# Kernel tuning notes

Hardware: AMD Instinct MI355X
Metric: run time of the kernel (lower is better)

The kernel has to match this reference:

```python
import jax, jax.numpy as jnp
import numpy as np

N_FEAT = 512
N_HEAD = 8
CONTEXT_SIZES = (31, 61)
HEADS_PER_SCALE = N_HEAD // len(CONTEXT_SIZES)  # 4
B, T = 4, 2048


def _windows(v, cs):
    """Gather overlapping local windows (faithful to chunkwise with N_c=1).
    v: [B, T, D] -> [B, T, cs, D], zero-padded at both ends by (cs-1)//2."""
    Bv, Tv, D = v.shape
    half = (cs - 1) // 2
    vp = jnp.pad(v, ((0, 0), (half, half), (0, 0)))
    idx = jnp.arange(Tv)[:, None] + jnp.arange(cs)[None, :]  # [T, cs]
    return vp[:, idx, :]


def setup_inputs() -> dict:
    key0 = jax.random.key(0)
    ks = jax.random.split(key0, 12)
    s = 0.02
    inp = {
        "query": jax.random.normal(ks[0], (B, T, N_FEAT), jnp.float32),
        "key": jax.random.normal(ks[1], (B, T, N_FEAT), jnp.float32),
        "value": jax.random.normal(ks[2], (B, T, N_FEAT), jnp.float32),
        # Linear weights stored torch-style [out_features, in_features]
        "w1_0": jax.random.normal(ks[3], (N_FEAT, N_FEAT), jnp.float32) * s,
        "w1_1": jax.random.normal(ks[4], (N_FEAT, N_FEAT), jnp.float32) * s,
        "w2_0": jax.random.normal(ks[5], (HEADS_PER_SCALE * CONTEXT_SIZES[0], N_FEAT), jnp.float32) * s,
        "w2_1": jax.random.normal(ks[6], (HEADS_PER_SCALE * CONTEXT_SIZES[1], N_FEAT), jnp.float32) * s,
        "w3_0": jax.random.normal(ks[7], (N_FEAT, N_FEAT), jnp.float32) * s,
        "w3_1": jax.random.normal(ks[8], (N_FEAT, N_FEAT), jnp.float32) * s,
        "scale_weights": jnp.ones((len(CONTEXT_SIZES),), jnp.float32) / len(CONTEXT_SIZES),
        "w_out": jax.random.normal(ks[9], (N_FEAT, N_FEAT), jnp.float32) * s,
    }
    return inp


def reference(query, key, value, w1_0, w1_1, w2_0, w2_1, w3_0, w3_1, scale_weights, w_out):
    # key is unused by the original module's forward.
    Bq, Tq, Fq = query.shape
    hd = Fq // N_HEAD  # per-head dim within a scale after splitting n_feat by heads_per_scale? No:
    head_dim = Fq // HEADS_PER_SCALE  # matches original: D // heads_per_scale
    outs = []
    for (w1, w2, w3, cs) in ((w1_0, w2_0, w3_0, CONTEXT_SIZES[0]),
                             (w1_1, w2_1, w3_1, CONTEXT_SIZES[1])):
        q = query @ w1.T                      # [B,T,F]
        v = value @ w3.T                      # [B,T,F]
        logits = jax.nn.relu(q) @ w2.T        # [B,T,HS*cs]
        attn = jax.nn.softmax(logits.reshape(Bq, Tq, HEADS_PER_SCALE, cs), axis=-1)
        # local windows of v: [B,T,cs,F] -> [B,T,cs,HS,head_dim]
        vw = _windows(v, cs).reshape(Bq, Tq, cs, HEADS_PER_SCALE, head_dim)
        x = jnp.einsum('bthc,btchd->bthd', attn, vw).reshape(Bq, Tq, Fq)
        outs.append(x)
    sw = jax.nn.softmax(scale_weights)
    x = sw[0] * outs[0] + sw[1] * outs[1]
    return x @ w_out.T
```

## Files before the change

kernel.cpp:

```cpp
#include <hip/hip_runtime.h>

typedef unsigned short u16;
typedef unsigned long long u64;
typedef float floatx4 __attribute__((ext_vector_type(4)));
typedef short shortx8 __attribute__((ext_vector_type(8)));

__device__ inline u16 f2bf(float f) {
  unsigned u = __float_as_uint(f);
  u += 0x7fffu + ((u >> 16) & 1u);
  return (u16)(u >> 16);
}

__device__ __forceinline__ void gl16(const u16* g, const u16* l) {
  __builtin_amdgcn_global_load_lds(
      (const __attribute__((address_space(1))) unsigned int*)(u64)(const void*)g,
      (__attribute__((address_space(3))) unsigned int*)(unsigned)(u64)(const void*)l,
      16, 0, 0);
}

__global__ __launch_bounds__(256) void convert_all(
    const float* __restrict__ q, const float* __restrict__ v,
    const float* __restrict__ w10, const float* __restrict__ w11,
    const float* __restrict__ w30, const float* __restrict__ w31,
    const float* __restrict__ wo, const float* __restrict__ w20,
    const float* __restrict__ w21, u16* __restrict__ base) {
  size_t e = ((size_t)blockIdx.x * 256 + threadIdx.x) * 4;
  const float* src;
  u16* dst;
  size_t le;
  unsigned prows;
  if (e < 4194304ull)      { src = q;   dst = base;            le = e;            prows = 0x7fffffffu; }
  else if (e < 8388608ull) { src = v;   dst = base + 4194304;  le = e - 4194304;  prows = 0x7fffffffu; }
  else if (e < 8650752ull) { src = w10; dst = base + 8388608;  le = e - 8388608;  prows = 0x7fffffffu; }
  else if (e < 8912896ull) { src = w11; dst = base + 8650752;  le = e - 8650752;  prows = 0x7fffffffu; }
  else if (e < 9175040ull) { src = w30; dst = base + 8912896;  le = e - 8912896;  prows = 0x7fffffffu; }
  else if (e < 9437184ull) { src = w31; dst = base + 9175040;  le = e - 9175040;  prows = 0x7fffffffu; }
  else if (e < 9699328ull) { src = wo;  dst = base + 9437184;  le = e - 9437184;  prows = 0x7fffffffu; }
  else if (e < 9764864ull) { src = w20; dst = base + 9699328;  le = e - 9699328;  prows = 124; }
  else                     { src = w21; dst = base + 9764864;  le = e - 9764864;  prows = 244; }
  float4 val = make_float4(0.f, 0.f, 0.f, 0.f);
  if ((unsigned)(le >> 9) < prows) val = *(const float4*)(src + le);
  unsigned p0 = (unsigned)f2bf(val.x) | ((unsigned)f2bf(val.y) << 16);
  unsigned p1 = (unsigned)f2bf(val.z) | ((unsigned)f2bf(val.w) << 16);
  *(uint2*)(dst + le) = make_uint2(p0, p1);
}

template <int OUTBF>
__device__ __forceinline__ void gemm_core(
    const u16* __restrict__ A, int lda, const u16* __restrict__ W, int ldw,
    float* __restrict__ Cf, u16* __restrict__ Cb, int ldc, int relu,
    u16* lA, u16* lB) {
  const int tid = threadIdx.x;
  const int wave = tid >> 6, lane = tid & 63;
  const int wm = (wave >> 1) * 64, wn = (wave & 1) * 64;
  const int lr = lane & 15, kq = (lane >> 4) * 8;
  const int sr = lane >> 2, sc = (lane & 3) * 8;

  floatx4 acc[4][4];
#pragma unroll
  for (int i = 0; i < 4; ++i)
#pragma unroll
    for (int j = 0; j < 4; ++j) acc[i][j] = (floatx4){0.f, 0.f, 0.f, 0.f};

  const u16* ga0 = A + (u64)(wave * 32 + sr) * lda + sc;
  const u16* ga1 = A + (u64)(wave * 32 + 16 + sr) * lda + sc;
  const u16* gb0 = W + (u64)(wave * 32 + sr) * ldw + sc;
  const u16* gb1 = W + (u64)(wave * 32 + 16 + sr) * ldw + sc;
  u16* la0 = lA + (wave * 32) * 32;
  u16* la1 = lA + (wave * 32 + 16) * 32;
  u16* lb0 = lB + (wave * 32) * 32;
  u16* lb1 = lB + (wave * 32 + 16) * 32;

  for (int k0 = 0; k0 < 512; k0 += 32) {
    __syncthreads();
    gl16(ga0 + k0, la0);
    gl16(ga1 + k0, la1);
    gl16(gb0 + k0, lb0);
    gl16(gb1 + k0, lb1);
    __syncthreads();
    shortx8 af[4], bf8[4];
#pragma unroll
    for (int i = 0; i < 4; ++i) {
      af[i] = *(const shortx8*)&lA[(wm + i * 16 + lr) * 32 + kq];
      bf8[i] = *(const shortx8*)&lB[(wn + i * 16 + lr) * 32 + kq];
    }
#pragma unroll
    for (int mi = 0; mi < 4; ++mi)
#pragma unroll
      for (int ni = 0; ni < 4; ++ni)
        acc[mi][ni] = __builtin_amdgcn_mfma_f32_16x16x32_bf16(af[mi], bf8[ni], acc[mi][ni], 0, 0, 0);
  }
  const int er = wm + (lane >> 4) * 4;
  const int ec = wn + lr;
#pragma unroll
  for (int mi = 0; mi < 4; ++mi)
#pragma unroll
    for (int ni = 0; ni < 4; ++ni)
#pragma unroll
      for (int r = 0; r < 4; ++r) {
        float vv = acc[mi][ni][r];
        if (relu) vv = fmaxf(vv, 0.f);
        u64 off = (u64)(er + mi * 16 + r) * (u64)ldc + (u64)(ec + ni * 16);
        if (OUTBF) Cb[off] = f2bf(vv);
        else Cf[off] = vv;
      }
}

__global__ __launch_bounds__(512, 2) void k_qv8(
    const u16* __restrict__ qb, const u16* __restrict__ vb,
    const u16* __restrict__ w1, const u16* __restrict__ w3,
    u16* __restrict__ rq, u16* __restrict__ vc) {
  extern __shared__ __align__(16) u16 lds[];
  const int bid = blockIdx.x;
  const int bx = (bid & 7) * 32 + (bid >> 3);
  const bool isq = bx < 128;
  const int lb = isq ? bx : bx - 128;
  const int m0 = (lb >> 2) * 256;
  const int n0 = (lb & 3) * 256;
  const u16* __restrict__ A = isq ? qb : vb;
  const u16* __restrict__ W = isq ? w1 : w3;
  u16* __restrict__ C = isq ? rq : vc;

  const int tid = threadIdx.x;
  const int wv = tid >> 6, lane = tid & 63;
  const int wr = wv >> 2, wc = wv & 3;
  const int lr = lane & 15, kq = lane >> 4;

  const unsigned Ca = ((unsigned)((lr >> 1) & 7)) << 3;
  const unsigned afb = ((unsigned)((wr * 128 + lr) * 32 + kq * 8)) ^ Ca;
  const unsigned bfb = ((unsigned)((wc * 32 + lr) * 32 + kq * 8)) ^ Ca;

  const unsigned u0 = (unsigned)(wv * 1024 + lane * 8);
  const unsigned u1 = u0 + 512;
  const unsigned g0 = u0 ^ (((u0 >> 6) & 7) << 3);
  const unsigned g1 = u1 ^ (((u1 >> 6) & 7) << 3);
  const unsigned gA0 = (unsigned)(m0 + (int)(g0 >> 5)) * 512u + (g0 & 31);
  const unsigned gA1 = (unsigned)(m0 + (int)(g1 >> 5)) * 512u + (g1 & 31);
  const unsigned rp0 = (g0 >> 5) & 127, rp1 = (g1 >> 5) & 127;
  const unsigned gB0n0 = (unsigned)(n0 + (int)((rp0 >> 5) * 64 + (rp0 & 31))) * 512u
                         + (g0 >> 12) * 32 + (g0 & 31);
  const unsigned gB1n0 = (unsigned)(n0 + (int)((rp1 >> 5) * 64 + (rp1 & 31))) * 512u
                         + (g1 >> 12) * 32 + (g1 & 31);
  const unsigned gB0n1 = gB0n0 + 32u * 512u;
  const unsigned gB1n1 = gB1n0 + 32u * 512u;
  const unsigned wvo = (unsigned)wv * 1024u;

#define SA(d, kk, ga, gb, ko) \
  gl16(A + (ga) + (ko), lds + (d)*16384 + (kk)*8192 + wvo); \
  gl16(A + (gb) + (ko), lds + (d)*16384 + (kk)*8192 + wvo + 512)
#define SB(d, nh, ga, gb, ko) \
  gl16(W + (ga) + (ko), lds + 32768 + (d)*16384 + (nh)*8192 + wvo); \
  gl16(W + (gb) + (ko), lds + 32768 + (d)*16384 + (nh)*8192 + wvo + 512)
#define LOAD_AF(kk, d) \
  _Pragma("unroll") \
  for (int m = 0; m < 8; ++m) \
    af[m] = *(const shortx8*)&lds[(d)*16384 + (kk)*8192 + afb + (unsigned)m * 512]
#define LOAD_BF(kk, nh, d) \
  bf0 = *(const shortx8*)&lds[32768 + (d)*16384 + (nh)*8192 + (kk)*4096 + bfb]; \
  bf1 = *(const shortx8*)&lds[32768 + (d)*16384 + (nh)*8192 + (kk)*4096 + bfb + 512]
#define MFMA16(nh) \
  __builtin_amdgcn_s_setprio(1); \
  _Pragma("unroll") \
  for (int m = 0; m < 8; ++m) { \
    acc[m][(nh)*2]   = __builtin_amdgcn_mfma_f32_16x16x32_bf16(af[m], bf0, acc[m][(nh)*2], 0, 0, 0); \
    acc[m][(nh)*2+1] = __builtin_amdgcn_mfma_f32_16x16x32_bf16(af[m], bf1, acc[m][(nh)*2+1], 0, 0, 0); \
  } \
  __builtin_amdgcn_s_setprio(0)
#define BAR() \
  __builtin_amdgcn_sched_barrier(0); \
  __builtin_amdgcn_s_barrier(); \
  asm volatile("" ::: "memory"); \
  __builtin_amdgcn_sched_barrier(0)
#define WAITVM4() \
  __builtin_amdgcn_sched_barrier(0); \
  asm volatile("s_waitcnt vmcnt(4)" ::: "memory"); \
  __builtin_amdgcn_sched_barrier(0)
#define WAITVM0() \
  __builtin_amdgcn_sched_barrier(0); \
  asm volatile("s_waitcnt vmcnt(0)" ::: "memory"); \
  __builtin_amdgcn_sched_barrier(0)

  floatx4 acc[8][4];
#pragma unroll
  for (int m = 0; m < 8; ++m)
#pragma unroll
    for (int n = 0; n < 4; ++n) acc[m][n] = (floatx4){0.f, 0.f, 0.f, 0.f};
  shortx8 af[8], bf0, bf1;

  SA(0, 0, gA0, gA1, 0);
  SB(0, 0, gB0n0, gB1n0, 0);
  SA(0, 1, gA0 + 32, gA1 + 32, 0);
  SB(0, 1, gB0n1, gB1n1, 0);
  SA(1, 0, gA0, gA1, 64);
  SB(1, 0, gB0n0, gB1n0, 64);
  WAITVM4();
  BAR();

#pragma unroll 1
  for (int i = 0; i < 3; ++i) {
    const unsigned k1 = (unsigned)(2 * i + 1) * 64u;
    const unsigned k2 = k1 + 64u, k3 = k1 + 128u;
    SA(1, 1, gA0 + 32, gA1 + 32, k1);
    LOAD_AF(0, 0); LOAD_BF(0, 0, 0); MFMA16(0);
    BAR();
    SB(1, 1, gB0n1, gB1n1, k1);
    LOAD_BF(0, 1, 0); MFMA16(1);
    BAR();
    SA(0, 0, gA0, gA1, k2);
    LOAD_AF(1, 0); LOAD_BF(1, 0, 0); MFMA16(0);
    BAR();
    SB(0, 0, gB0n0, gB1n0, k2);
    LOAD_BF(1, 1, 0); MFMA16(1);
    WAITVM4();
    BAR();
    SA(0, 1, gA0 + 32, gA1 + 32, k2);
    LOAD_AF(0, 1); LOAD_BF(0, 0, 1); MFMA16(0);
    BAR();
    SB(0, 1, gB0n1, gB1n1, k2);
    LOAD_BF(0, 1, 1); MFMA16(1);
    BAR();
    SA(1, 0, gA0, gA1, k3);
    LOAD_AF(1, 1); LOAD_BF(1, 0, 1); MFMA16(0);
    BAR();
    SB(1, 0, gB0n0, gB1n0, k3);
    LOAD_BF(1, 1, 1); MFMA16(1);
    WAITVM4();
    BAR();
  }
  {
    const unsigned k1 = 448u;
    SA(1, 1, gA0 + 32, gA1 + 32, k1);
    LOAD_AF(0, 0); LOAD_BF(0, 0, 0); MFMA16(0);
    BAR();
    SB(1, 1, gB0n1, gB1n1, k1);
    LOAD_BF(0, 1, 0); MFMA16(1);
    BAR();
    LOAD_AF(1, 0); LOAD_BF(1, 0, 0); MFMA16(0);
    BAR();
    LOAD_BF(1, 1, 0); MFMA16(1);
    WAITVM0();
    BAR();
    LOAD_AF(0, 1); LOAD_BF(0, 0, 1); MFMA16(0);
    BAR();
    LOAD_BF(0, 1, 1); MFMA16(1);
    BAR();
    LOAD_AF(1, 1); LOAD_BF(1, 0, 1); MFMA16(0);
    BAR();
    LOAD_BF(1, 1, 1); MFMA16(1);
  }

  const int er0 = m0 + wr * 128 + (lane >> 4) * 4;
  const int ec0 = n0 + wc * 64 + lr;
#pragma unroll
  for (int m = 0; m < 8; ++m)
#pragma unroll
    for (int n = 0; n < 4; ++n)
#pragma unroll
      for (int r = 0; r < 4; ++r) {
        float vv = acc[m][n][r];
        if (isq) vv = fmaxf(vv, 0.f);
        C[(u64)(er0 + m * 16 + r) * 1024 + (u64)(ec0 + n * 16)] = f2bf(vv);
      }
#undef SA
#undef SB
#undef LOAD_AF
#undef LOAD_BF
#undef MFMA16
#undef BAR
#undef WAITVM4
#undef WAITVM0
}

__global__ __launch_bounds__(256, 2) void k_logits(
    const u16* __restrict__ rq, const u16* __restrict__ w20,
    const u16* __restrict__ w21, float* __restrict__ lg) {
  __shared__ __align__(16) u16 lA[128 * 32];
  __shared__ __align__(16) u16 lB[128 * 32];
  const int am = blockIdx.x * 128;
  const int y = blockIdx.y;
  const u16* A = rq + (u64)am * 1024 + (y == 0 ? 0 : 512);
  const u16* W = (y == 0) ? w20 : (w21 + (u64)(y - 1) * 128 * 512);
  float* Cf = lg + (u64)am * 384 + y * 128;
  gemm_core<0>(A, 1024, W, 512, Cf, nullptr, 384, 0, lA, lB);
}

__global__ __launch_bounds__(256, 2) void k_final(
    const u16* __restrict__ xb, const u16* __restrict__ wo,
    float* __restrict__ out) {
  __shared__ __align__(16) u16 lA[128 * 32];
  __shared__ __align__(16) u16 lB[128 * 32];
  const int am = blockIdx.x * 128, bn = blockIdx.y * 128;
  gemm_core<0>(xb + (u64)am * 512, 512, wo + (u64)bn * 512, 512,
               out + (u64)am * 512 + bn, nullptr, 512, 0, lA, lB);
}

#define VLDT 136
#define ESL 152

template <int CS, int CHUNK>
__device__ __forceinline__ void attn_mfma_pass(
    const float* __restrict__ lg,
    const u16* __restrict__ vbh,
    int bb, int t0, float swv,
    u16* vT, u16* es16, float* invsum, floatx4 (&o)[4]) {
  constexpr int HALF = (CS - 1) / 2;
  constexpr int NW = 64 + CS - 1;
  const int tid = threadIdx.x;
  const int wave = tid >> 6, lane = tid & 63;
  const int lr = lane & 15, kq = (lane >> 4) * 8;

  __syncthreads();

#pragma unroll
  for (int it = 0; it < 4; ++it) {
    int idx = it * 256 + tid;
    int r = idx >> 3;
    int dl8 = (idx & 7) * 8;
    int t = t0 + r - HALF;
    uint4 u = make_uint4(0u, 0u, 0u, 0u);
    if (r < NW && t >= 0 && t < 2048)
      u = *(const uint4*)&vbh[(u64)(bb + t) * 1024 + dl8];
    int sb = (((r >> 3) ^ ((dl8 >> 3) & 7)) << 3) + (r & 7);
    u16* wp = &vT[dl8 * VLDT + sb];
    const u16* us = (const u16*)&u;
#pragma unroll
    for (int j = 0; j < 8; ++j) wp[j * VLDT] = us[j];
  }

  {
    int tt = tid >> 2, qq = tid & 3;
    u16* row = es16 + tt * ESL;
    const int lo = tt, hi = tt + CS;
#pragma unroll
    for (int j = 0; j < 32; ++j) {
      int x = qq * 32 + j;
      if (x < lo || x >= hi) row[x] = 0;
    }
    const float* lrow = lg + (u64)(bb + t0 + tt) * 384 + qq * CHUNK;
    float ps = 0.f;
#pragma unroll
    for (int j = 0; j < CHUNK; ++j) {
      int c = qq * CHUNK + j;
      if (c < CS) {
        float ev = __expf(lrow[j]);
        row[lo + c] = f2bf(ev);
        ps += ev;
      }
    }
    ps += __shfl_xor(ps, 1, 64);
    ps += __shfl_xor(ps, 2, 64);
    if (qq == 0) invsum[tt] = swv / ps;
  }
  __syncthreads();

  const int kb_lo = (wave * 16) >> 5;
  const int kb_hi = (wave * 16 + 15 + CS - 1) >> 5;
  floatx4 acc[4];
#pragma unroll
  for (int nt = 0; nt < 4; ++nt) acc[nt] = (floatx4){0.f, 0.f, 0.f, 0.f};
  for (int kb = kb_lo; kb <= kb_hi; ++kb) {
    shortx8 af = *(const shortx8*)&es16[(wave * 16 + lr) * ESL + kb * 32 + kq];
    int rb8 = kb * 4 + (lane >> 4);
#pragma unroll
    for (int nt = 0; nt < 4; ++nt) {
      int d_row = nt * 16 + lr;
      int blk = (rb8 ^ ((d_row >> 3) & 7)) << 3;
      shortx8 bf8 = *(const shortx8*)&vT[d_row * VLDT + blk];
      acc[nt] = __builtin_amdgcn_mfma_f32_16x16x32_bf16(af, bf8, acc[nt], 0, 0, 0);
    }
  }
  float invs[4];
#pragma unroll
  for (int rr = 0; rr < 4; ++rr)
    invs[rr] = invsum[wave * 16 + (lane >> 4) * 4 + rr];
#pragma unroll
  for (int nt = 0; nt < 4; ++nt)
#pragma unroll
    for (int rr = 0; rr < 4; ++rr) o[nt][rr] += acc[nt][rr] * invs[rr];
}

__global__ __launch_bounds__(256, 2) void k_attn4(
    const float* __restrict__ lg, const u16* __restrict__ vcat,
    const float* __restrict__ swp, u16* __restrict__ xbw) {
  __shared__ __align__(16) u16 vT[64 * VLDT];
  __shared__ __align__(16) u16 es16[64 * ESL];
  __shared__ float invsum[64];
  const int tid = threadIdx.x;
  const int wave = tid >> 6, lane = tid & 63;
  const int lr = lane & 15;
  const int t0 = blockIdx.x * 64;
  const int h = blockIdx.y >> 1, dh = blockIdx.y & 1;
  const int b = blockIdx.z;
  const int bb = b * 2048;
  const int m0 = bb + t0;

  float a0 = swp[0], a1 = swp[1];
  float mx = fmaxf(a0, a1);
  float e0 = __expf(a0 - mx), e1 = __expf(a1 - mx);
  float inv = 1.f / (e0 + e1);

  floatx4 o[4];
#pragma unroll
  for (int nt = 0; nt < 4; ++nt) o[nt] = (floatx4){0.f, 0.f, 0.f, 0.f};

  attn_mfma_pass<31, 8>(lg + h * 31, vcat + h * 128 + dh * 64,
                        bb, t0, e0 * inv, vT, es16, invsum, o);
  attn_mfma_pass<61, 16>(lg + 128 + h * 61, vcat + 512 + h * 128 + dh * 64,
                         bb, t0, e1 * inv, vT, es16, invsum, o);

  __syncthreads();
#pragma unroll
  for (int nt = 0; nt < 4; ++nt)
#pragma unroll
    for (int rr = 0; rr < 4; ++rr) {
      int trow = wave * 16 + (lane >> 4) * 4 + rr;
      es16[trow * ESL + nt * 16 + lr] = f2bf(o[nt][rr]);
    }
  __syncthreads();
#pragma unroll
  for (int rep = 0; rep < 2; ++rep) {
    int idx = rep * 256 + tid;
    int trow = idx >> 3;
    int col8 = (idx & 7) * 8;
    uint4 u = *(const uint4*)&es16[trow * ESL + col8];
    *(uint4*)&xbw[(u64)(m0 + trow) * 512 + h * 128 + dh * 64 + col8] = u;
  }
}

extern "C" void kernel_launch(void* const* d_in, const int* in_sizes, int n_in,
                              void* d_out, int out_size, void* d_ws, size_t ws_size,
                              hipStream_t stream) {
  const float* q   = (const float*)d_in[0];
  const float* v   = (const float*)d_in[2];
  const float* w10 = (const float*)d_in[3];
  const float* w11 = (const float*)d_in[4];
  const float* w20 = (const float*)d_in[5];
  const float* w21 = (const float*)d_in[6];
  const float* w30 = (const float*)d_in[7];
  const float* w31 = (const float*)d_in[8];
  const float* sw  = (const float*)d_in[9];
  const float* wo  = (const float*)d_in[10];
  float* out = (float*)d_out;

  u16* base  = (u16*)d_ws;
  u16* qb    = base;
  u16* vb    = base + 4194304;
  u16* w1cat = base + 8388608;
  u16* w3cat = base + 8912896;
  u16* wob   = base + 9437184;
  u16* w2b0  = base + 9699328;
  u16* w2b1  = base + 9764864;
  char* fb = (char*)d_ws + 19791872;
  float* logitsC = (float*)fb;
  u16* rqcat = (u16*)(logitsC + 3145728);
  u16* vcat  = rqcat + 8388608;
  u16* xb    = vcat + 8388608;

  static bool attr_done = false;
  if (!attr_done) {
    hipFuncSetAttribute((const void*)k_qv8,
                        hipFuncAttributeMaxDynamicSharedMemorySize, 131072);
    attr_done = true;
  }

  convert_all<<<dim3(9664), dim3(256), 0, stream>>>(q, v, w10, w11, w30, w31, wo, w20, w21, base);

  dim3 blk(256);
  k_qv8<<<dim3(256), dim3(512), 131072, stream>>>(qb, vb, w1cat, w3cat, rqcat, vcat);
  k_logits<<<dim3(64, 3), blk, 0, stream>>>(rqcat, w2b0, w2b1, logitsC);
  k_attn4<<<dim3(32, 8, 4), blk, 0, stream>>>(logitsC, vcat, sw, xb);
  k_final<<<dim3(64, 4), blk, 0, stream>>>(xb, wob, out);
}
```

Measured before the change: 169.8 us.

## Fuse fp32-to-bf16 conversion of query/value into the projection GEMM loader

Drops the separate conversion of query and value activations from the convert kernel. The QV projection GEMM now reads fp32 rows directly into registers, packs them to bf16 and writes them into swizzled LDS, with a reworked vmcnt/lgkmcnt wait schedule and dummy loads to keep the counters aligned. This removes a full write and re-read of the bf16 activation copies. In exchange the A-operand path moves from async global-to-LDS loads to register-staged loads with conversion ALU work inside the main loop.

```diff
diff --git a/kernel.cpp b/kernel.cpp
--- a/kernel.cpp
+++ b/kernel.cpp
@@ -19,7 +19,6 @@
 }
 
 __global__ __launch_bounds__(256) void convert_all(
-    const float* __restrict__ q, const float* __restrict__ v,
     const float* __restrict__ w10, const float* __restrict__ w11,
     const float* __restrict__ w30, const float* __restrict__ w31,
     const float* __restrict__ wo, const float* __restrict__ w20,
@@ -29,15 +28,13 @@
   u16* dst;
   size_t le;
   unsigned prows;
-  if (e < 4194304ull)      { src = q;   dst = base;            le = e;            prows = 0x7fffffffu; }
-  else if (e < 8388608ull) { src = v;   dst = base + 4194304;  le = e - 4194304;  prows = 0x7fffffffu; }
-  else if (e < 8650752ull) { src = w10; dst = base + 8388608;  le = e - 8388608;  prows = 0x7fffffffu; }
-  else if (e < 8912896ull) { src = w11; dst = base + 8650752;  le = e - 8650752;  prows = 0x7fffffffu; }
-  else if (e < 9175040ull) { src = w30; dst = base + 8912896;  le = e - 8912896;  prows = 0x7fffffffu; }
-  else if (e < 9437184ull) { src = w31; dst = base + 9175040;  le = e - 9175040;  prows = 0x7fffffffu; }
-  else if (e < 9699328ull) { src = wo;  dst = base + 9437184;  le = e - 9437184;  prows = 0x7fffffffu; }
-  else if (e < 9764864ull) { src = w20; dst = base + 9699328;  le = e - 9699328;  prows = 124; }
-  else                     { src = w21; dst = base + 9764864;  le = e - 9764864;  prows = 244; }
+  if (e < 262144ull)        { src = w10; dst = base + 8388608; le = e;            prows = 0x7fffffffu; }
+  else if (e < 524288ull)   { src = w11; dst = base + 8650752; le = e - 262144;   prows = 0x7fffffffu; }
+  else if (e < 786432ull)   { src = w30; dst = base + 8912896; le = e - 524288;   prows = 0x7fffffffu; }
+  else if (e < 1048576ull)  { src = w31; dst = base + 9175040; le = e - 786432;   prows = 0x7fffffffu; }
+  else if (e < 1310720ull)  { src = wo;  dst = base + 9437184; le = e - 1048576;  prows = 0x7fffffffu; }
+  else if (e < 1376256ull)  { src = w20; dst = base + 9699328; le = e - 1310720;  prows = 124; }
+  else                      { src = w21; dst = base + 9764864; le = e - 1376256;  prows = 244; }
   float4 val = make_float4(0.f, 0.f, 0.f, 0.f);
   if ((unsigned)(le >> 9) < prows) val = *(const float4*)(src + le);
   unsigned p0 = (unsigned)f2bf(val.x) | ((unsigned)f2bf(val.y) << 16);
@@ -107,7 +104,7 @@
 }
 
 __global__ __launch_bounds__(512, 2) void k_qv8(
-    const u16* __restrict__ qb, const u16* __restrict__ vb,
+    const float* __restrict__ qf, const float* __restrict__ vf,
     const u16* __restrict__ w1, const u16* __restrict__ w3,
     u16* __restrict__ rq, u16* __restrict__ vc) {
   extern __shared__ __align__(16) u16 lds[];
@@ -117,7 +114,7 @@
   const int lb = isq ? bx : bx - 128;
   const int m0 = (lb >> 2) * 256;
   const int n0 = (lb & 3) * 256;
-  const u16* __restrict__ A = isq ? qb : vb;
+  const float* __restrict__ Af = isq ? qf : vf;
   const u16* __restrict__ W = isq ? w1 : w3;
   u16* __restrict__ C = isq ? rq : vc;
 
@@ -134,8 +131,6 @@
   const unsigned u1 = u0 + 512;
   const unsigned g0 = u0 ^ (((u0 >> 6) & 7) << 3);
   const unsigned g1 = u1 ^ (((u1 >> 6) & 7) << 3);
-  const unsigned gA0 = (unsigned)(m0 + (int)(g0 >> 5)) * 512u + (g0 & 31);
-  const unsigned gA1 = (unsigned)(m0 + (int)(g1 >> 5)) * 512u + (g1 & 31);
   const unsigned rp0 = (g0 >> 5) & 127, rp1 = (g1 >> 5) & 127;
   const unsigned gB0n0 = (unsigned)(n0 + (int)((rp0 >> 5) * 64 + (rp0 & 31))) * 512u
                          + (g0 >> 12) * 32 + (g0 & 31);
@@ -145,12 +140,27 @@
   const unsigned gB1n1 = gB1n0 + 32u * 512u;
   const unsigned wvo = (unsigned)wv * 1024u;
 
-#define SA(d, kk, ga, gb, ko) \
-  gl16(A + (ga) + (ko), lds + (d)*16384 + (kk)*8192 + wvo); \
-  gl16(A + (gb) + (ko), lds + (d)*16384 + (kk)*8192 + wvo + 512)
+  const float* ap = Af + (u64)(m0 + (tid >> 1)) * 512 + (unsigned)(tid & 1) * 16u;
+  const unsigned u0a = (unsigned)tid * 16u;
+  const unsigned xA = ((u0a >> 6) & 7u) << 3;
+  const unsigned puA0 = u0a ^ xA;
+  const unsigned puA1 = (u0a + 8u) ^ xA;
+
 #define SB(d, nh, ga, gb, ko) \
   gl16(W + (ga) + (ko), lds + 32768 + (d)*16384 + (nh)*8192 + wvo); \
   gl16(W + (gb) + (ko), lds + 32768 + (d)*16384 + (nh)*8192 + wvo + 512)
+#define ISSA(s, koff) { \
+  const uint4* p_ = (const uint4*)(ap + (koff)); \
+  s[0] = p_[0]; s[1] = p_[1]; s[2] = p_[2]; s[3] = p_[3]; }
+#define PKU(a, b) ((unsigned)f2bf(__uint_as_float(a)) | ((unsigned)f2bf(__uint_as_float(b)) << 16))
+#define WRA(s, d, kk) { \
+  uint4 w0_, w1_; \
+  w0_.x = PKU(s[0].x, s[0].y); w0_.y = PKU(s[0].z, s[0].w); \
+  w0_.z = PKU(s[1].x, s[1].y); w0_.w = PKU(s[1].z, s[1].w); \
+  w1_.x = PKU(s[2].x, s[2].y); w1_.y = PKU(s[2].z, s[2].w); \
+  w1_.z = PKU(s[3].x, s[3].y); w1_.w = PKU(s[3].z, s[3].w); \
+  *(uint4*)&lds[(d)*16384 + (kk)*8192 + puA0] = w0_; \
+  *(uint4*)&lds[(d)*16384 + (kk)*8192 + puA1] = w1_; }
 #define LOAD_AF(kk, d) \
   _Pragma("unroll") \
   for (int m = 0; m < 8; ++m) \
@@ -166,19 +176,40 @@
     acc[m][(nh)*2+1] = __builtin_amdgcn_mfma_f32_16x16x32_bf16(af[m], bf1, acc[m][(nh)*2+1], 0, 0, 0); \
   } \
   __builtin_amdgcn_s_setprio(0)
+#define FENCE() asm volatile("" ::: "memory")
 #define BAR() \
   __builtin_amdgcn_sched_barrier(0); \
   __builtin_amdgcn_s_barrier(); \
   asm volatile("" ::: "memory"); \
   __builtin_amdgcn_sched_barrier(0)
-#define WAITVM4() \
+#define LGKM0() \
+  __builtin_amdgcn_sched_barrier(0); \
+  asm volatile("s_waitcnt lgkmcnt(0)" ::: "memory"); \
+  __builtin_amdgcn_sched_barrier(0)
+#define VM0() \
+  __builtin_amdgcn_sched_barrier(0); \
+  asm volatile("s_waitcnt vmcnt(0)" ::: "memory"); \
+  __builtin_amdgcn_sched_barrier(0)
+#define VM4() \
   __builtin_amdgcn_sched_barrier(0); \
   asm volatile("s_waitcnt vmcnt(4)" ::: "memory"); \
   __builtin_amdgcn_sched_barrier(0)
-#define WAITVM0() \
-  __builtin_amdgcn_sched_barrier(0); \
-  asm volatile("s_waitcnt vmcnt(0)" ::: "memory"); \
-  __builtin_amdgcn_sched_barrier(0)
+#define VM6() \
+  __builtin_amdgcn_sched_barrier(0); \
+  asm volatile("s_waitcnt vmcnt(6)" ::: "memory"); \
+  __builtin_amdgcn_sched_barrier(0)
+#define VM8() \
+  __builtin_amdgcn_sched_barrier(0); \
+  asm volatile("s_waitcnt vmcnt(8)" ::: "memory"); \
+  __builtin_amdgcn_sched_barrier(0)
+#define VM12() \
+  __builtin_amdgcn_sched_barrier(0); \
+  asm volatile("s_waitcnt vmcnt(12)" ::: "memory"); \
+  __builtin_amdgcn_sched_barrier(0)
+#define DUMMY2() { \
+  volatile const unsigned* dp_ = (volatile const unsigned*)Af; \
+  unsigned t0_ = dp_[lane]; unsigned t1_ = dp_[lane + 64]; \
+  asm volatile("" :: "v"(t0_), "v"(t1_)); }
 
   floatx4 acc[8][4];
 #pragma unroll
@@ -186,60 +217,72 @@
 #pragma unroll
     for (int n = 0; n < 4; ++n) acc[m][n] = (floatx4){0.f, 0.f, 0.f, 0.f};
   shortx8 af[8], bf0, bf1;
-
-  SA(0, 0, gA0, gA1, 0);
+  uint4 sa[4], sb[4];
+
+  ISSA(sa, 0u); FENCE();
+  ISSA(sb, 32u); FENCE();
+  VM4(); WRA(sa, 0, 0);
+  ISSA(sa, 64u); FENCE();
+  VM4(); WRA(sb, 0, 1);
+  VM0(); WRA(sa, 1, 0);
+  FENCE();
   SB(0, 0, gB0n0, gB1n0, 0);
-  SA(0, 1, gA0 + 32, gA1 + 32, 0);
   SB(0, 1, gB0n1, gB1n1, 0);
-  SA(1, 0, gA0, gA1, 64);
   SB(1, 0, gB0n0, gB1n0, 64);
-  WAITVM4();
+  FENCE();
+  ISSA(sa, 96u); FENCE();
+  DUMMY2(); FENCE();
+  ISSA(sb, 128u); FENCE();
+  DUMMY2(); FENCE();
+  VM12();
+  LGKM0();
   BAR();
 
 #pragma unroll 1
   for (int i = 0; i < 3; ++i) {
-    const unsigned k1 = (unsigned)(2 * i + 1) * 64u;
-    const unsigned k2 = k1 + 64u, k3 = k1 + 128u;
-    SA(1, 1, gA0 + 32, gA1 + 32, k1);
+    const unsigned ke = (unsigned)i * 128u;
+    const unsigned k1 = ke + 64u, k2 = ke + 128u, k3 = ke + 192u;
+    const unsigned k8 = (i == 2) ? 0u : ke + 256u;
+    VM8(); WRA(sa, 1, 1);
     LOAD_AF(0, 0); LOAD_BF(0, 0, 0); MFMA16(0);
-    BAR();
-    SB(1, 1, gB0n1, gB1n1, k1);
+    LGKM0(); BAR();
+    ISSA(sa, ke + 160u); FENCE();
+    SB(1, 1, gB0n1, gB1n1, k1); FENCE();
     LOAD_BF(0, 1, 0); MFMA16(1);
     BAR();
-    SA(0, 0, gA0, gA1, k2);
+    VM8(); WRA(sb, 0, 0);
     LOAD_AF(1, 0); LOAD_BF(1, 0, 0); MFMA16(0);
-    BAR();
-    SB(0, 0, gB0n0, gB1n0, k2);
+    LGKM0(); BAR();
+    ISSA(sb, ke + 192u); FENCE();
+    SB(0, 0, gB0n0, gB1n0, k2); FENCE();
     LOAD_BF(1, 1, 0); MFMA16(1);
-    WAITVM4();
-    BAR();
-    SA(0, 1, gA0 + 32, gA1 + 32, k2);
+    VM6(); BAR();
+    VM8(); WRA(sa, 0, 1);
     LOAD_AF(0, 1); LOAD_BF(0, 0, 1); MFMA16(0);
-    BAR();
-    SB(0, 1, gB0n1, gB1n1, k2);
+    LGKM0(); BAR();
+    ISSA(sa, ke + 224u); FENCE();
+    SB(0, 1, gB0n1, gB1n1, k2); FENCE();
     LOAD_BF(0, 1, 1); MFMA16(1);
     BAR();
-    SA(1, 0, gA0, gA1, k3);
+    VM8(); WRA(sb, 1, 0);
     LOAD_AF(1, 1); LOAD_BF(1, 0, 1); MFMA16(0);
-    BAR();
-    SB(1, 0, gB0n0, gB1n0, k3);
+    LGKM0(); BAR();
+    ISSA(sb, k8); FENCE();
+    SB(1, 0, gB0n0, gB1n0, k3); FENCE();
     LOAD_BF(1, 1, 1); MFMA16(1);
-    WAITVM4();
-    BAR();
+    VM6(); BAR();
   }
   {
-    const unsigned k1 = 448u;
-    SA(1, 1, gA0 + 32, gA1 + 32, k1);
+    VM8(); WRA(sa, 1, 1);
     LOAD_AF(0, 0); LOAD_BF(0, 0, 0); MFMA16(0);
-    BAR();
-    SB(1, 1, gB0n1, gB1n1, k1);
+    LGKM0(); BAR();
+    SB(1, 1, gB0n1, gB1n1, 448); FENCE();
     LOAD_BF(0, 1, 0); MFMA16(1);
     BAR();
     LOAD_AF(1, 0); LOAD_BF(1, 0, 0); MFMA16(0);
     BAR();
     LOAD_BF(1, 1, 0); MFMA16(1);
-    WAITVM0();
-    BAR();
+    VM0(); BAR();
     LOAD_AF(0, 1); LOAD_BF(0, 0, 1); MFMA16(0);
     BAR();
     LOAD_BF(0, 1, 1); MFMA16(1);
@@ -261,14 +304,22 @@
         if (isq) vv = fmaxf(vv, 0.f);
         C[(u64)(er0 + m * 16 + r) * 1024 + (u64)(ec0 + n * 16)] = f2bf(vv);
       }
-#undef SA
 #undef SB
+#undef ISSA
+#undef PKU
+#undef WRA
 #undef LOAD_AF
 #undef LOAD_BF
 #undef MFMA16
+#undef FENCE
 #undef BAR
-#undef WAITVM4
-#undef WAITVM0
+#undef LGKM0
+#undef VM0
+#undef VM4
+#undef VM6
+#undef VM8
+#undef VM12
+#undef DUMMY2
 }
 
 __global__ __launch_bounds__(256, 2) void k_logits(
@@ -443,8 +494,6 @@
   float* out = (float*)d_out;
 
   u16* base  = (u16*)d_ws;
-  u16* qb    = base;
-  u16* vb    = base + 4194304;
   u16* w1cat = base + 8388608;
   u16* w3cat = base + 8912896;
   u16* wob   = base + 9437184;
@@ -463,10 +512,10 @@
     attr_done = true;
   }
 
-  convert_all<<<dim3(9664), dim3(256), 0, stream>>>(q, v, w10, w11, w30, w31, wo, w20, w21, base);
+  convert_all<<<dim3(1472), dim3(256), 0, stream>>>(w10, w11, w30, w31, wo, w20, w21, base);
 
   dim3 blk(256);
-  k_qv8<<<dim3(256), dim3(512), 131072, stream>>>(qb, vb, w1cat, w3cat, rqcat, vcat);
+  k_qv8<<<dim3(256), dim3(512), 131072, stream>>>(q, v, w1cat, w3cat, rqcat, vcat);
   k_logits<<<dim3(64, 3), blk, 0, stream>>>(rqcat, w2b0, w2b1, logitsC);
   k_attn4<<<dim3(32, 8, 4), blk, 0, stream>>>(logitsC, vcat, sw, xb);
   k_final<<<dim3(64, 4), blk, 0, stream>>>(xb, wob, out);
```

New measurement: 197.4 us. +16.3%, slower.
